# Kernel tuning notes

Measured on AMD Instinct MI355X. Metric: run time of the kernel, lower is better.

The kernel has to match this reference:

```python
import jax, jax.numpy as jnp
import numpy as np

P = 3  # patch_size
EPS = 1e-12  # F.normalize default eps (denom = max(norm, eps))


def setup_inputs() -> dict:
    key = jax.random.key(0)
    k1, k2 = jax.random.split(key)
    B, C, H, W, D = 2, 32, 96, 160, 32
    q = jax.random.normal(k1, (B, C, H, W), dtype=jnp.float32)
    warped_feat = jax.random.normal(k2, (B, C, H, W, D), dtype=jnp.float32)
    return {"q": q, "warped_feat": warped_feat}


def reference(q, warped_feat):
    # q: [B,C,H,W]; warped_feat: [B,C,H,W,D]
    # Equivalent to: unfold PxP patches around each pixel (zero pad),
    # L2-normalize the C*P*P patch vector per pixel, then cosine dot
    # between the q patch and each of D warped-feature patches.
    # Computed shift-by-shift to avoid materializing the C*P*P unfold.
    B, C, H, W = q.shape
    D = warped_feat.shape[-1]
    pad = P // 2
    qp = jnp.pad(q, ((0, 0), (0, 0), (pad, pad), (pad, pad)))
    kp = jnp.pad(warped_feat, ((0, 0), (0, 0), (pad, pad), (pad, pad), (0, 0)))

    dot = jnp.zeros((B, H, W, D), dtype=q.dtype)
    q2 = jnp.zeros((B, H, W), dtype=q.dtype)
    k2 = jnp.zeros((B, H, W, D), dtype=q.dtype)
    for dy in range(P):
        for dx in range(P):
            qs = qp[:, :, dy:dy + H, dx:dx + W]            # [B,C,H,W]
            ks = kp[:, :, dy:dy + H, dx:dx + W, :]         # [B,C,H,W,D]
            dot = dot + jnp.einsum('bchw,bchwd->bhwd', qs, ks)
            q2 = q2 + jnp.sum(qs * qs, axis=1)
            k2 = k2 + jnp.sum(ks * ks, axis=1)

    nq = jnp.maximum(jnp.sqrt(q2), EPS)[..., None]         # [B,H,W,1]
    nk = jnp.maximum(jnp.sqrt(k2), EPS)                    # [B,H,W,D]
    sim = dot / (nq * nk)                                  # [B,H,W,D]
    return jnp.transpose(sim, (0, 3, 1, 2))                # [B,D,H,W]
```

## Files before the change

### kernel.cpp

```cpp
#include <hip/hip_runtime.h>

constexpr int B = 2, C = 32, H = 96, W = 160, D = 32;
constexpr int HW = H * W;
constexpr int NP = B * H * W;
constexpr float EPS = 1e-12f;

__global__ __launch_bounds__(256) void dav_stage1(
    const float* __restrict__ q, const float* __restrict__ k,
    float* __restrict__ s, float* __restrict__ nk, float* __restrict__ nq) {
  int gt = blockIdx.x * 256 + threadIdx.x;
  int pixel = gt >> 3;
  int dg = gt & 7;
  if (pixel >= NP) return;
  int b  = pixel / HW;
  int hw = pixel - b * HW;

  const float* kbase = k + ((size_t)b * C * HW + hw) * D + dg * 4;
  const float* qbase = q + (size_t)b * C * HW + hw;

  float4 s4 = make_float4(0.f, 0.f, 0.f, 0.f);
  float4 n4 = make_float4(0.f, 0.f, 0.f, 0.f);
  float  nqv = 0.f;

#pragma unroll
  for (int c = 0; c < C; ++c) {
    float4 k4 = *reinterpret_cast<const float4*>(kbase + (size_t)c * HW * D);
    float  qc = qbase[(size_t)c * HW];
    s4.x = fmaf(qc, k4.x, s4.x);
    s4.y = fmaf(qc, k4.y, s4.y);
    s4.z = fmaf(qc, k4.z, s4.z);
    s4.w = fmaf(qc, k4.w, s4.w);
    n4.x = fmaf(k4.x, k4.x, n4.x);
    n4.y = fmaf(k4.y, k4.y, n4.y);
    n4.z = fmaf(k4.z, k4.z, n4.z);
    n4.w = fmaf(k4.w, k4.w, n4.w);
    nqv  = fmaf(qc, qc, nqv);
  }

  int d0 = dg * 4;
  size_t obase = ((size_t)b * D + d0) * HW + hw;
  s[obase]          = s4.x;
  s[obase + HW]     = s4.y;
  s[obase + 2 * HW] = s4.z;
  s[obase + 3 * HW] = s4.w;
  nk[obase]          = n4.x;
  nk[obase + HW]     = n4.y;
  nk[obase + 2 * HW] = n4.z;
  nk[obase + 3 * HW] = n4.w;
  if (dg == 0) nq[pixel] = nqv;
}

__global__ __launch_bounds__(256) void dav_stage2(
    const float* __restrict__ s, const float* __restrict__ nk,
    const float* __restrict__ nq, float* __restrict__ out) {
  int idx = blockIdx.x * 256 + threadIdx.x;
  if (idx >= B * D * HW) return;
  int w  = idx % W;
  int h  = (idx / W) % H;
  int bd = idx / HW;
  int b  = bd / D;

  const float* srow = s  + (size_t)bd * HW;
  const float* nrow = nk + (size_t)bd * HW;
  const float* qrow = nq + (size_t)b * HW;

  float dot = 0.f, k2 = 0.f, q2 = 0.f;
#pragma unroll
  for (int dy = -1; dy <= 1; ++dy) {
    int hh = h + dy;
    if (hh < 0 || hh >= H) continue;
#pragma unroll
    for (int dx = -1; dx <= 1; ++dx) {
      int ww = w + dx;
      if (ww < 0 || ww >= W) continue;
      int off = hh * W + ww;
      dot += srow[off];
      k2  += nrow[off];
      q2  += qrow[off];
    }
  }
  float dq = fmaxf(sqrtf(q2), EPS);
  float dk = fmaxf(sqrtf(k2), EPS);
  out[idx] = dot / (dq * dk);
}

extern "C" void kernel_launch(void* const* d_in, const int* in_sizes, int n_in,
                              void* d_out, int out_size, void* d_ws, size_t ws_size,
                              hipStream_t stream) {
  const float* q = (const float*)d_in[0];
  const float* k = (const float*)d_in[1];
  float* out = (float*)d_out;

  float* s  = (float*)d_ws;
  float* nk = s + (size_t)NP * D;
  float* nq = nk + (size_t)NP * D;

  {
    int threads = NP * 8;
    int blocks = (threads + 255) / 256;
    dav_stage1<<<blocks, 256, 0, stream>>>(q, k, s, nk, nq);
  }
  {
    int n = B * D * HW;
    int blocks = (n + 255) / 256;
    dav_stage2<<<blocks, 256, 0, stream>>>(s, nk, nq, out);
  }
}
```

Measured before the change: 38.57 us.

## Interleave dot and norm partials, precompute q box norm, 4-wide stage2

Stage 1 now writes the per-pixel dot and k-norm partials as interleaved float2 pairs instead of two separate arrays. A new small kernel box-sums the q norms once per pixel and stores the reciprocal norm, so stage 2 no longer repeats that sum for every D. Stage 2 has each thread produce four adjacent outputs from shared column sums and write them with one float4 store. This cuts redundant neighbour loads, at the cost of an extra kernel launch and fewer threads in stage 2.

```diff
diff --git a/kernel.cpp b/kernel.cpp
--- a/kernel.cpp
+++ b/kernel.cpp
@@ -3,11 +3,12 @@
 constexpr int B = 2, C = 32, H = 96, W = 160, D = 32;
 constexpr int HW = H * W;
 constexpr int NP = B * H * W;
+constexpr int WG = W / 4;
 constexpr float EPS = 1e-12f;
 
 __global__ __launch_bounds__(256) void dav_stage1(
     const float* __restrict__ q, const float* __restrict__ k,
-    float* __restrict__ s, float* __restrict__ nk, float* __restrict__ nq) {
+    float2* __restrict__ sn, float* __restrict__ nq) {
   int gt = blockIdx.x * 256 + threadIdx.x;
   int pixel = gt >> 3;
   int dg = gt & 7;
@@ -15,8 +16,8 @@
   int b  = pixel / HW;
   int hw = pixel - b * HW;
 
-  const float* kbase = k + ((size_t)b * C * HW + hw) * D + dg * 4;
-  const float* qbase = q + (size_t)b * C * HW + hw;
+  const float* kbase = k + ((size_t)(b * C) * HW + hw) * D + dg * 4;
+  const float* qbase = q + (size_t)(b * C) * HW + hw;
 
   float4 s4 = make_float4(0.f, 0.f, 0.f, 0.f);
   float4 n4 = make_float4(0.f, 0.f, 0.f, 0.f);
@@ -37,34 +38,23 @@
     nqv  = fmaf(qc, qc, nqv);
   }
 
-  int d0 = dg * 4;
-  size_t obase = ((size_t)b * D + d0) * HW + hw;
-  s[obase]          = s4.x;
-  s[obase + HW]     = s4.y;
-  s[obase + 2 * HW] = s4.z;
-  s[obase + 3 * HW] = s4.w;
-  nk[obase]          = n4.x;
-  nk[obase + HW]     = n4.y;
-  nk[obase + 2 * HW] = n4.z;
-  nk[obase + 3 * HW] = n4.w;
+  size_t obase = ((size_t)(b * D + dg * 4)) * HW + hw;
+  sn[obase]          = make_float2(s4.x, n4.x);
+  sn[obase + HW]     = make_float2(s4.y, n4.y);
+  sn[obase + 2 * HW] = make_float2(s4.z, n4.z);
+  sn[obase + 3 * HW] = make_float2(s4.w, n4.w);
   if (dg == 0) nq[pixel] = nqv;
 }
 
-__global__ __launch_bounds__(256) void dav_stage2(
-    const float* __restrict__ s, const float* __restrict__ nk,
-    const float* __restrict__ nq, float* __restrict__ out) {
-  int idx = blockIdx.x * 256 + threadIdx.x;
-  if (idx >= B * D * HW) return;
-  int w  = idx % W;
-  int h  = (idx / W) % H;
-  int bd = idx / HW;
-  int b  = bd / D;
-
-  const float* srow = s  + (size_t)bd * HW;
-  const float* nrow = nk + (size_t)bd * HW;
-  const float* qrow = nq + (size_t)b * HW;
-
-  float dot = 0.f, k2 = 0.f, q2 = 0.f;
+__global__ __launch_bounds__(256) void dav_nqbox(
+    const float* __restrict__ nq, float* __restrict__ rq) {
+  int p = blockIdx.x * 256 + threadIdx.x;
+  if (p >= NP) return;
+  int w = p % W;
+  int h = (p / W) % H;
+  int b = p / HW;
+  const float* base = nq + (size_t)b * HW;
+  float acc = 0.f;
 #pragma unroll
   for (int dy = -1; dy <= 1; ++dy) {
     int hh = h + dy;
@@ -73,15 +63,54 @@
     for (int dx = -1; dx <= 1; ++dx) {
       int ww = w + dx;
       if (ww < 0 || ww >= W) continue;
-      int off = hh * W + ww;
-      dot += srow[off];
-      k2  += nrow[off];
-      q2  += qrow[off];
+      acc += base[hh * W + ww];
     }
   }
-  float dq = fmaxf(sqrtf(q2), EPS);
-  float dk = fmaxf(sqrtf(k2), EPS);
-  out[idx] = dot / (dq * dk);
+  rq[p] = 1.f / fmaxf(sqrtf(acc), EPS);
+}
+
+__global__ __launch_bounds__(256) void dav_stage2(
+    const float2* __restrict__ sn, const float* __restrict__ rq,
+    float* __restrict__ out) {
+  int idx = blockIdx.x * 256 + threadIdx.x;
+  if (idx >= B * D * H * WG) return;
+  int g  = idx % WG;
+  int h  = (idx / WG) % H;
+  int bd = idx / (WG * H);
+  int b  = bd / D;
+  int w0 = g * 4;
+
+  float csS[6] = {0.f, 0.f, 0.f, 0.f, 0.f, 0.f};
+  float csN[6] = {0.f, 0.f, 0.f, 0.f, 0.f, 0.f};
+  const float2* plane = sn + (size_t)bd * HW;
+#pragma unroll
+  for (int r = -1; r <= 1; ++r) {
+    int hh = h + r;
+    if (hh < 0 || hh >= H) continue;
+    const float2* row = plane + hh * W;
+#pragma unroll
+    for (int i = 0; i < 6; ++i) {
+      int c = w0 - 1 + i;
+      if (c >= 0 && c < W) {
+        float2 v = row[c];
+        csS[i] += v.x;
+        csN[i] += v.y;
+      }
+    }
+  }
+
+  float4 rq4 = *reinterpret_cast<const float4*>(rq + (size_t)b * HW + h * W + w0);
+  const float* rqa = &rq4.x;
+  float o[4];
+#pragma unroll
+  for (int i = 0; i < 4; ++i) {
+    float dot = csS[i] + csS[i + 1] + csS[i + 2];
+    float k2  = csN[i] + csN[i + 1] + csN[i + 2];
+    float dk  = fmaxf(sqrtf(k2), EPS);
+    o[i] = dot * rqa[i] / dk;
+  }
+  *reinterpret_cast<float4*>(out + (size_t)bd * HW + h * W + w0) =
+      make_float4(o[0], o[1], o[2], o[3]);
 }
 
 extern "C" void kernel_launch(void* const* d_in, const int* in_sizes, int n_in,
@@ -91,18 +120,22 @@
   const float* k = (const float*)d_in[1];
   float* out = (float*)d_out;
 
-  float* s  = (float*)d_ws;
-  float* nk = s + (size_t)NP * D;
-  float* nq = nk + (size_t)NP * D;
+  float2* sn = (float2*)d_ws;
+  float*  nq = (float*)(sn + (size_t)NP * D);
+  float*  rq = nq + NP;
 
   {
     int threads = NP * 8;
     int blocks = (threads + 255) / 256;
-    dav_stage1<<<blocks, 256, 0, stream>>>(q, k, s, nk, nq);
+    dav_stage1<<<blocks, 256, 0, stream>>>(q, k, sn, nq);
   }
   {
-    int n = B * D * HW;
+    int blocks = (NP + 255) / 256;
+    dav_nqbox<<<blocks, 256, 0, stream>>>(nq, rq);
+  }
+  {
+    int n = B * D * H * WG;
     int blocks = (n + 255) / 256;
-    dav_stage2<<<blocks, 256, 0, stream>>>(s, nk, nq, out);
+    dav_stage2<<<blocks, 256, 0, stream>>>(sn, rq, out);
   }
 }
```

Measured after the change: 38.03 us. No clear change (-1.4%).
